# Performance work log

Measured on AMD Instinct MI355X. Metric: run time of the kernel, lower is better.

## Reference

```python
import jax, jax.numpy as jnp
import numpy as np

S, B, I, H = 2048, 128, 128, 128


def setup_inputs() -> dict:
    key = jax.random.key(0)
    k1, k2, k3, k4, k5 = jax.random.split(key, 5)
    x = jax.random.normal(k1, (S, B, I), dtype=jnp.float32)
    V = jax.random.normal(k2, (4 * H, I), dtype=jnp.float32) * 0.05
    W = jax.random.normal(k3, (4 * H, H), dtype=jnp.float32) * 0.05
    b = jax.random.normal(k4, (4 * H,), dtype=jnp.float32) * 0.05
    b2 = jax.random.normal(k5, (4 * H,), dtype=jnp.float32) * 0.05
    return {"x": x, "V": V, "W": W, "b": b, "b2": b2}


def reference(x, V, W, b, b2):
    seq_len, batch, _ = x.shape
    hid = W.shape[1]
    # Precompute input contribution for all timesteps (same math, batched matmul)
    xg = jnp.einsum('sbi,gi->sbg', x, V) + b + b2  # (S, B, 4H)

    def step(carry, xg_t):
        h, c = carry
        gates = xg_t + h @ W.T  # (B, 4H)
        i, f, g, o = jnp.split(gates, 4, axis=1)
        i = jax.nn.sigmoid(i)
        f = jax.nn.sigmoid(f)
        g = jnp.tanh(g)
        o = jax.nn.sigmoid(o)
        c = f * c + i * g
        h = o * jnp.tanh(c)
        return (h, c), h

    h0 = jnp.zeros((batch, hid), dtype=x.dtype)
    c0 = jnp.zeros((batch, hid), dtype=x.dtype)
    (h_T, c_T), hs = jax.lax.scan(step, (h0, c0), xg)  # hs: (S, B, H)
    # Original torch.cat of h_t.unsqueeze(1) along dim 0 -> (S*B, 1, H)
    h_seq = hs.reshape(seq_len * batch, 1, hid)
    return h_seq, h_T[:, None, :], c_T[:, None, :]
```

## Files before the change

### kernel.cpp

```cpp
#include <hip/hip_runtime.h>
#include <hip/hip_bf16.h>
#include <hip/hip_fp16.h>


#define S_LEN 2048
#define BATCH 128
#define HID   128
#define G4    512

typedef _Float16 h2_t __attribute__((ext_vector_type(2)));
typedef _Float16 h8_t __attribute__((ext_vector_type(8)));
typedef float    f4_t __attribute__((ext_vector_type(4)));

__global__ __launch_bounds__(256, 2)
void xg_gemm(const float* __restrict__ x, const float* __restrict__ V,
             const float* __restrict__ b, const float* __restrict__ b2,
             __half* __restrict__ xg)
{
    __shared__ h8_t As[128 * 16];
    __shared__ h8_t Bs[128 * 16];

    const int t  = threadIdx.x;
    const int m0 = blockIdx.y * 128;
    const int n0 = blockIdx.x * 128;

#pragma unroll
    for (int r = 0; r < 8; ++r) {
        int id  = t + 256 * r;
        int row = id >> 4;
        int j   = id & 15;
        const float4* gx = (const float4*)(x + (long)(m0 + row) * 128 + j * 8);
        float4 a0 = gx[0], a1 = gx[1];
        h8_t ha = { (_Float16)a0.x, (_Float16)a0.y, (_Float16)a0.z, (_Float16)a0.w,
                    (_Float16)a1.x, (_Float16)a1.y, (_Float16)a1.z, (_Float16)a1.w };
        As[row * 16 + (j ^ (row & 15))] = ha;
        const float4* gv = (const float4*)(V + (long)(n0 + row) * 128 + j * 8);
        float4 b0 = gv[0], b1 = gv[1];
        h8_t hb = { (_Float16)b0.x, (_Float16)b0.y, (_Float16)b0.z, (_Float16)b0.w,
                    (_Float16)b1.x, (_Float16)b1.y, (_Float16)b1.z, (_Float16)b1.w };
        Bs[row * 16 + (j ^ (row & 15))] = hb;
    }
    __syncthreads();

    const int w    = t >> 6;
    const int lane = t & 63;
    const int m    = lane & 15;
    const int quad = lane >> 4;

    f4_t acc[2][8];
#pragma unroll
    for (int i = 0; i < 2; ++i)
#pragma unroll
        for (int j = 0; j < 8; ++j) acc[i][j] = (f4_t)0.f;

#pragma unroll
    for (int ks = 0; ks < 4; ++ks) {
        int ch = ks * 4 + quad;
        h8_t a0 = As[(w * 32      + m) * 16 + (ch ^ m)];
        h8_t a1 = As[(w * 32 + 16 + m) * 16 + (ch ^ m)];
#pragma unroll
        for (int nt = 0; nt < 8; ++nt) {
            h8_t bf = Bs[(nt * 16 + m) * 16 + (ch ^ m)];
            acc[0][nt] = __builtin_amdgcn_mfma_f32_16x16x32_f16(a0, bf, acc[0][nt], 0, 0, 0);
            acc[1][nt] = __builtin_amdgcn_mfma_f32_16x16x32_f16(a1, bf, acc[1][nt], 0, 0, 0);
        }
    }

#pragma unroll
    for (int nt = 0; nt < 8; ++nt) {
        int col = n0 + nt * 16 + m;
        float bias = b[col] + b2[col];
#pragma unroll
        for (int mi = 0; mi < 2; ++mi) {
#pragma unroll
            for (int rg = 0; rg < 4; ++rg) {
                long mrow = (long)(m0 + w * 32 + mi * 16 + quad * 4 + rg);
                xg[mrow * G4 + col] = __float2half(acc[mi][nt][rg] + bias);
            }
        }
    }
}

__device__ __forceinline__ float fsig(float x) {
    return __builtin_amdgcn_rcpf(1.f + __expf(-x));
}
__device__ __forceinline__ float ftanh(float x) {
    return 1.f - 2.f * __builtin_amdgcn_rcpf(1.f + __expf(2.f * x));
}
__device__ __forceinline__ void bar() {
    asm volatile("s_waitcnt lgkmcnt(0)" ::: "memory");
    __builtin_amdgcn_s_barrier();
    asm volatile("" ::: "memory");
}

__global__ __launch_bounds__(512, 2)
void lstm_scan(const __half* __restrict__ xg, const float* __restrict__ W,
               float* __restrict__ out)
{
    const int bidx = blockIdx.x;
    const int t    = threadIdx.x;
    const int w    = t >> 6;
    const int lane = t & 63;
    const int col  = lane & 15;
    const int quad = lane >> 4;
    const int rg   = col & 3;
    const int hid  = 16 * w + quad * 4 + rg;

    __shared__ __align__(16) __half h_buf[2][HID];

    h8_t a[4][4];
#pragma unroll
    for (int g = 0; g < 4; ++g) {
        const float* Wr = W + (long)(g * 128 + 16 * w + col) * 128 + quad * 8;
#pragma unroll
        for (int kc = 0; kc < 4; ++kc) {
            const float4* wp = (const float4*)(Wr + kc * 32);
            float4 v0 = wp[0], v1 = wp[1];
            a[g][kc] = h8_t{ (_Float16)v0.x, (_Float16)v0.y, (_Float16)v0.z, (_Float16)v0.w,
                             (_Float16)v1.x, (_Float16)v1.y, (_Float16)v1.z, (_Float16)v1.w };
        }
    }

    if (t < HID) h_buf[0][t] = __float2half(0.f);
    __syncthreads();

    const __half* xp = xg + (long)bidx * G4 + hid;
    const long step_stride = (long)BATCH * G4;

    __half p[4][4];
#pragma unroll
    for (int j = 0; j < 4; ++j) {
        const __half* q = xp + (long)j * step_stride;
#pragma unroll
        for (int g = 0; g < 4; ++g) p[j][g] = q[g * 128];
    }

    float c = 0.f, hlast = 0.f;
    float* outp = out + (long)bidx * HID + hid;
    const long SBH = (long)S_LEN * BATCH * HID;

    const bool sel1 = (col & 1) != 0;
    const bool sel2 = (col & 2) != 0;

    for (int s0 = 0; s0 < S_LEN; s0 += 4) {
#pragma unroll
        for (int u = 0; u < 4; ++u) {
            const int s = s0 + u;

            float xv0 = __half2float(p[u][0]);
            float xv1 = __half2float(p[u][1]);
            float xv2 = __half2float(p[u][2]);
            float xv3 = __half2float(p[u][3]);

            {
                int sn = s + 4; sn = (sn < S_LEN) ? sn : (S_LEN - 1);
                const __half* q = xp + (long)sn * step_stride;
                p[u][0] = q[0];
                p[u][1] = q[128];
                p[u][2] = q[256];
                p[u][3] = q[384];
            }

            const h8_t* hb = (const h8_t*)(&h_buf[s & 1][0]);

            f4_t acc0 = (f4_t)0.f, acc1 = (f4_t)0.f, acc2 = (f4_t)0.f, acc3 = (f4_t)0.f;
#pragma unroll
            for (int kc = 0; kc < 4; ++kc) {
                h8_t bf = hb[kc * 4 + quad];
                acc0 = __builtin_amdgcn_mfma_f32_16x16x32_f16(a[0][kc], bf, acc0, 0, 0, 0);
                acc1 = __builtin_amdgcn_mfma_f32_16x16x32_f16(a[1][kc], bf, acc1, 0, 0, 0);
                acc2 = __builtin_amdgcn_mfma_f32_16x16x32_f16(a[2][kc], bf, acc2, 0, 0, 0);
                acc3 = __builtin_amdgcn_mfma_f32_16x16x32_f16(a[3][kc], bf, acc3, 0, 0, 0);
            }

            float v01, v23;
            v01 = sel1 ? acc0[1] : acc0[0];  v23 = sel1 ? acc0[3] : acc0[2];
            float pi = (sel2 ? v23 : v01) + xv0;
            v01 = sel1 ? acc1[1] : acc1[0];  v23 = sel1 ? acc1[3] : acc1[2];
            float pf = (sel2 ? v23 : v01) + xv1;
            v01 = sel1 ? acc2[1] : acc2[0];  v23 = sel1 ? acc2[3] : acc2[2];
            float pg = (sel2 ? v23 : v01) + xv2;
            v01 = sel1 ? acc3[1] : acc3[0];  v23 = sel1 ? acc3[3] : acc3[2];
            float po = (sel2 ? v23 : v01) + xv3;

            float ia = fsig(pi);
            float fa = fsig(pf);
            float ga = ftanh(pg);
            float oa = fsig(po);
            c = fa * c + ia * ga;
            float hv = oa * ftanh(c);
            hlast = hv;

            if (col < 4) {
                h_buf[(s + 1) & 1][hid] = __float2half(hv);
                *outp = hv;
            }
            outp += BATCH * HID;
            bar();
        }
    }

    if (col < 4) {
        out[SBH + (long)bidx * HID + hid]                     = hlast;
        out[SBH + (long)BATCH * HID + (long)bidx * HID + hid] = c;
    }
}

extern "C" void kernel_launch(void* const* d_in, const int* in_sizes, int n_in,
                              void* d_out, int out_size, void* d_ws, size_t ws_size,
                              hipStream_t stream) {
    const float* x  = (const float*)d_in[0];
    const float* V  = (const float*)d_in[1];
    const float* W  = (const float*)d_in[2];
    const float* b  = (const float*)d_in[3];
    const float* b2 = (const float*)d_in[4];
    float* out = (float*)d_out;
    __half* xg = (__half*)d_ws;

    dim3 g1(G4 / 128, (S_LEN * BATCH) / 128);
    xg_gemm<<<g1, dim3(256), 0, stream>>>(x, V, b, b2, xg);
    lstm_scan<<<dim3(BATCH), dim3(512), 0, stream>>>(xg, W, out);
}
```

Baseline: 1.379 ms.

## Stage xg in double-buffered LDS chunks and fold bias into MFMA accumulators

The scan kernel no longer issues four scalar half-precision global loads per step. Each block now copies 16-step chunks of its xg rows into a double-buffered shared-memory tile with wide vector loads, prefetching two chunks ahead and writing the next buffer just before each chunk's last barrier. The bias add moves out of the GEMM epilogue: the fp32 bias seeds the recurrent MFMA accumulators, and the h fragments are read up front. This aims to take global-load latency and issue overhead off the serial per-step path, at the cost of extra LDS reads, about 32KB of shared memory per block, and chunk-boundary store work.

```diff
diff --git a/kernel.cpp b/kernel.cpp
--- a/kernel.cpp
+++ b/kernel.cpp
@@ -8,13 +8,13 @@
 #define HID   128
 #define G4    512
 
-typedef _Float16 h2_t __attribute__((ext_vector_type(2)));
 typedef _Float16 h8_t __attribute__((ext_vector_type(8)));
 typedef float    f4_t __attribute__((ext_vector_type(4)));
 
+#define MFMA16(A, B, C) __builtin_amdgcn_mfma_f32_16x16x32_f16((A), (B), (C), 0, 0, 0)
+
 __global__ __launch_bounds__(256, 2)
 void xg_gemm(const float* __restrict__ x, const float* __restrict__ V,
-             const float* __restrict__ b, const float* __restrict__ b2,
              __half* __restrict__ xg)
 {
     __shared__ h8_t As[128 * 16];
@@ -61,21 +61,20 @@
 #pragma unroll
         for (int nt = 0; nt < 8; ++nt) {
             h8_t bf = Bs[(nt * 16 + m) * 16 + (ch ^ m)];
-            acc[0][nt] = __builtin_amdgcn_mfma_f32_16x16x32_f16(a0, bf, acc[0][nt], 0, 0, 0);
-            acc[1][nt] = __builtin_amdgcn_mfma_f32_16x16x32_f16(a1, bf, acc[1][nt], 0, 0, 0);
+            acc[0][nt] = MFMA16(a0, bf, acc[0][nt]);
+            acc[1][nt] = MFMA16(a1, bf, acc[1][nt]);
         }
     }
 
 #pragma unroll
     for (int nt = 0; nt < 8; ++nt) {
         int col = n0 + nt * 16 + m;
-        float bias = b[col] + b2[col];
 #pragma unroll
         for (int mi = 0; mi < 2; ++mi) {
 #pragma unroll
             for (int rg = 0; rg < 4; ++rg) {
                 long mrow = (long)(m0 + w * 32 + mi * 16 + quad * 4 + rg);
-                xg[mrow * G4 + col] = __float2half(acc[mi][nt][rg] + bias);
+                xg[mrow * G4 + col] = __float2half(acc[mi][nt][rg]);
             }
         }
     }
@@ -93,8 +92,12 @@
     asm volatile("" ::: "memory");
 }
 
+#define CHUNK 16
+#define NCHUNK (S_LEN / CHUNK)
+
 __global__ __launch_bounds__(512, 2)
 void lstm_scan(const __half* __restrict__ xg, const float* __restrict__ W,
+               const float* __restrict__ b, const float* __restrict__ b2,
                float* __restrict__ out)
 {
     const int bidx = blockIdx.x;
@@ -106,6 +109,7 @@
     const int rg   = col & 3;
     const int hid  = 16 * w + quad * 4 + rg;
 
+    __shared__ __align__(16) __half xgb[2][CHUNK][G4];
     __shared__ __align__(16) __half h_buf[2][HID];
 
     h8_t a[4][4];
@@ -115,72 +119,73 @@
 #pragma unroll
         for (int kc = 0; kc < 4; ++kc) {
             const float4* wp = (const float4*)(Wr + kc * 32);
-            float4 v0 = wp[0], v1 = wp[1];
-            a[g][kc] = h8_t{ (_Float16)v0.x, (_Float16)v0.y, (_Float16)v0.z, (_Float16)v0.w,
-                             (_Float16)v1.x, (_Float16)v1.y, (_Float16)v1.z, (_Float16)v1.w };
-        }
-    }
+            float4 w0 = wp[0], w1 = wp[1];
+            a[g][kc] = h8_t{ (_Float16)w0.x, (_Float16)w0.y, (_Float16)w0.z, (_Float16)w0.w,
+                             (_Float16)w1.x, (_Float16)w1.y, (_Float16)w1.z, (_Float16)w1.w };
+        }
+    }
+
+    f4_t bias4[4];
+#pragma unroll
+    for (int g = 0; g < 4; ++g)
+#pragma unroll
+        for (int r = 0; r < 4; ++r) {
+            int idx = g * 128 + 16 * w + quad * 4 + r;
+            bias4[g][r] = b[idx] + b2[idx];
+        }
+
+    const int r0 = w, r1 = w + 8;
+    const h8_t* src0 = (const h8_t*)(xg + ((long)r0 * BATCH + bidx) * G4 + lane * 8);
+    const h8_t* src1 = (const h8_t*)(xg + ((long)r1 * BATCH + bidx) * G4 + lane * 8);
+    const long chunk_stride = (long)CHUNK * BATCH * G4 / 8;
+
+    h8_t st0 = src0[0], st1 = src1[0];
+    *(h8_t*)(&xgb[0][r0][lane * 8]) = st0;
+    *(h8_t*)(&xgb[0][r1][lane * 8]) = st1;
+    st0 = src0[chunk_stride];
+    st1 = src1[chunk_stride];
 
     if (t < HID) h_buf[0][t] = __float2half(0.f);
     __syncthreads();
-
-    const __half* xp = xg + (long)bidx * G4 + hid;
-    const long step_stride = (long)BATCH * G4;
-
-    __half p[4][4];
-#pragma unroll
-    for (int j = 0; j < 4; ++j) {
-        const __half* q = xp + (long)j * step_stride;
-#pragma unroll
-        for (int g = 0; g < 4; ++g) p[j][g] = q[g * 128];
-    }
 
     float c = 0.f, hlast = 0.f;
     float* outp = out + (long)bidx * HID + hid;
     const long SBH = (long)S_LEN * BATCH * HID;
-
     const bool sel1 = (col & 1) != 0;
     const bool sel2 = (col & 2) != 0;
 
-    for (int s0 = 0; s0 < S_LEN; s0 += 4) {
-#pragma unroll
-        for (int u = 0; u < 4; ++u) {
-            const int s = s0 + u;
-
-            float xv0 = __half2float(p[u][0]);
-            float xv1 = __half2float(p[u][1]);
-            float xv2 = __half2float(p[u][2]);
-            float xv3 = __half2float(p[u][3]);
-
-            {
-                int sn = s + 4; sn = (sn < S_LEN) ? sn : (S_LEN - 1);
-                const __half* q = xp + (long)sn * step_stride;
-                p[u][0] = q[0];
-                p[u][1] = q[128];
-                p[u][2] = q[256];
-                p[u][3] = q[384];
-            }
-
-            const h8_t* hb = (const h8_t*)(&h_buf[s & 1][0]);
-
-            f4_t acc0 = (f4_t)0.f, acc1 = (f4_t)0.f, acc2 = (f4_t)0.f, acc3 = (f4_t)0.f;
-#pragma unroll
-            for (int kc = 0; kc < 4; ++kc) {
-                h8_t bf = hb[kc * 4 + quad];
-                acc0 = __builtin_amdgcn_mfma_f32_16x16x32_f16(a[0][kc], bf, acc0, 0, 0, 0);
-                acc1 = __builtin_amdgcn_mfma_f32_16x16x32_f16(a[1][kc], bf, acc1, 0, 0, 0);
-                acc2 = __builtin_amdgcn_mfma_f32_16x16x32_f16(a[2][kc], bf, acc2, 0, 0, 0);
-                acc3 = __builtin_amdgcn_mfma_f32_16x16x32_f16(a[3][kc], bf, acc3, 0, 0, 0);
-            }
+    for (int ch = 0; ch < NCHUNK; ++ch) {
+        const int buf = ch & 1;
+#pragma unroll
+        for (int sl = 0; sl < CHUNK; ++sl) {
+            const h8_t* hb = (const h8_t*)(&h_buf[sl & 1][0]);
+            h8_t hf0 = hb[quad], hf1 = hb[4 + quad], hf2 = hb[8 + quad],
+                 hf3 = hb[12 + quad];
+
+            const __half* xr = &xgb[buf][sl][hid];
+            float xv0 = __half2float(xr[0]);
+            float xv1 = __half2float(xr[128]);
+            float xv2 = __half2float(xr[256]);
+            float xv3 = __half2float(xr[384]);
+
+            f4_t g0 = bias4[0], g1 = bias4[1], g2 = bias4[2], g3 = bias4[3];
+            g0 = MFMA16(a[0][0], hf0, g0);  g1 = MFMA16(a[1][0], hf0, g1);
+            g2 = MFMA16(a[2][0], hf0, g2);  g3 = MFMA16(a[3][0], hf0, g3);
+            g0 = MFMA16(a[0][1], hf1, g0);  g1 = MFMA16(a[1][1], hf1, g1);
+            g2 = MFMA16(a[2][1], hf1, g2);  g3 = MFMA16(a[3][1], hf1, g3);
+            g0 = MFMA16(a[0][2], hf2, g0);  g1 = MFMA16(a[1][2], hf2, g1);
+            g2 = MFMA16(a[2][2], hf2, g2);  g3 = MFMA16(a[3][2], hf2, g3);
+            g0 = MFMA16(a[0][3], hf3, g0);  g1 = MFMA16(a[1][3], hf3, g1);
+            g2 = MFMA16(a[2][3], hf3, g2);  g3 = MFMA16(a[3][3], hf3, g3);
 
             float v01, v23;
-            v01 = sel1 ? acc0[1] : acc0[0];  v23 = sel1 ? acc0[3] : acc0[2];
+            v01 = sel1 ? g0[1] : g0[0];  v23 = sel1 ? g0[3] : g0[2];
             float pi = (sel2 ? v23 : v01) + xv0;
-            v01 = sel1 ? acc1[1] : acc1[0];  v23 = sel1 ? acc1[3] : acc1[2];
+            v01 = sel1 ? g1[1] : g1[0];  v23 = sel1 ? g1[3] : g1[2];
             float pf = (sel2 ? v23 : v01) + xv1;
-            v01 = sel1 ? acc2[1] : acc2[0];  v23 = sel1 ? acc2[3] : acc2[2];
+            v01 = sel1 ? g2[1] : g2[0];  v23 = sel1 ? g2[3] : g2[2];
             float pg = (sel2 ? v23 : v01) + xv2;
-            v01 = sel1 ? acc3[1] : acc3[0];  v23 = sel1 ? acc3[3] : acc3[2];
+            v01 = sel1 ? g3[1] : g3[0];  v23 = sel1 ? g3[3] : g3[2];
             float po = (sel2 ? v23 : v01) + xv3;
 
             float ia = fsig(pi);
@@ -192,10 +197,18 @@
             hlast = hv;
 
             if (col < 4) {
-                h_buf[(s + 1) & 1][hid] = __float2half(hv);
+                h_buf[(sl + 1) & 1][hid] = __float2half(hv);
                 *outp = hv;
             }
             outp += BATCH * HID;
+
+            if (sl == CHUNK - 1) {
+                *(h8_t*)(&xgb[buf ^ 1][r0][lane * 8]) = st0;
+                *(h8_t*)(&xgb[buf ^ 1][r1][lane * 8]) = st1;
+                long cn = (ch + 2 < NCHUNK) ? (ch + 2) : (NCHUNK - 1);
+                st0 = src0[cn * chunk_stride];
+                st1 = src1[cn * chunk_stride];
+            }
             bar();
         }
     }
@@ -218,6 +231,6 @@
     __half* xg = (__half*)d_ws;
 
     dim3 g1(G4 / 128, (S_LEN * BATCH) / 128);
-    xg_gemm<<<g1, dim3(256), 0, stream>>>(x, V, b, b2, xg);
-    lstm_scan<<<dim3(BATCH), dim3(512), 0, stream>>>(xg, W, out);
-}
+    xg_gemm<<<g1, dim3(256), 0, stream>>>(x, V, xg);
+    lstm_scan<<<dim3(BATCH), dim3(512), 0, stream>>>(xg, W, b, b2, out);
+}
```

Measured after the change: 1.378 ms. Within noise of the previous version (-0.1%).
